# Kernel tuning notes

Hardware: AMD Instinct MI355X
Metric: run time of the kernel (lower is better)

## Reference

```python
import jax, jax.numpy as jnp
import numpy as np

B, T, C, H, E, K = 4, 1024, 1024, 16, 8, 2
HID = 4 * C

def _ln(x, g, b, eps=1e-5):
    m = jnp.mean(x, -1, keepdims=True)
    v = jnp.mean((x - m) ** 2, -1, keepdims=True)
    return (x - m) * jax.lax.rsqrt(v + eps) * g + b

def setup_inputs() -> dict:
    key = jax.random.key(0)
    ks = jax.random.split(key, 8)
    s = 0.02
    return {
        "x": jax.random.normal(ks[0], (B, T, C), jnp.float32),
        "attention_mask": jnp.ones((B, T), jnp.int32),
        "Wq": jax.random.normal(ks[1], (C, C), jnp.float32) * s,
        "bq": jnp.zeros((C,), jnp.float32),
        "Wk": jax.random.normal(ks[2], (C, C), jnp.float32) * s,
        "bk": jnp.zeros((C,), jnp.float32),
        "Wv": jax.random.normal(ks[3], (C, C), jnp.float32) * s,
        "bv": jnp.zeros((C,), jnp.float32),
        "Wo": jax.random.normal(ks[4], (C, C), jnp.float32) * s,
        "bo": jnp.zeros((C,), jnp.float32),
        "ln1_g": jnp.ones((C,), jnp.float32),
        "ln1_b": jnp.zeros((C,), jnp.float32),
        "ln2_g": jnp.ones((C,), jnp.float32),
        "ln2_b": jnp.zeros((C,), jnp.float32),
        "Wr": jax.random.normal(ks[5], (C, E), jnp.float32) * s,
        "br": jnp.zeros((E,), jnp.float32),
        "W1": jax.random.normal(ks[6], (E, C, HID), jnp.float32) * s,
        "b1": jnp.zeros((E, HID), jnp.float32),
        "W2": jax.random.normal(ks[7], (E, HID, C), jnp.float32) * s,
        "b2": jnp.zeros((E, C), jnp.float32),
    }

def reference(x, attention_mask, Wq, bq, Wk, bk, Wv, bv, Wo, bo,
              ln1_g, ln1_b, ln2_g, ln2_b, Wr, br, W1, b1, W2, b2):
    b, t, c = x.shape
    d = c // H
    # --- multi-head self-attention with causal + padding mask ---
    q = (x @ Wq + bq).reshape(b, t, H, d).transpose(0, 2, 1, 3)  # bhtd
    k = (x @ Wk + bk).reshape(b, t, H, d).transpose(0, 2, 1, 3)
    v = (x @ Wv + bv).reshape(b, t, H, d).transpose(0, 2, 1, 3)
    scores = jnp.einsum('bhqd,bhkd->bhqk', q, k) * (1.0 / jnp.sqrt(jnp.float32(d)))
    causal = jnp.tril(jnp.ones((t, t), bool))[None, None]            # [1,1,T,T]
    mask = causal & (attention_mask[:, None, None, :] > 0)          # [B,1,T,T]
    scores = jnp.where(mask, scores, jnp.float32(-1e9))
    attn = jax.nn.softmax(scores, axis=-1)
    o = jnp.einsum('bhqk,bhkd->bhqd', attn, v).transpose(0, 2, 1, 3).reshape(b, t, c)
    mha_out = o @ Wo + bo
    x1 = _ln(x + mha_out, ln1_g, ln1_b)
    # --- sparse MoE: router -> top-k gates -> expert MLPs -> combine ---
    logits = x1 @ Wr + br                               # [B,T,E]
    probs = jax.nn.softmax(logits, axis=-1)
    _, topi = jax.lax.top_k(logits, K)                  # [B,T,K]
    emask = jnp.any(topi[..., None] == jnp.arange(E), axis=-2)  # [B,T,E] bool
    gates = jax.nn.softmax(jnp.where(emask, logits, jnp.float32(-1e9)), axis=-1)
    h = jax.nn.relu(jnp.einsum('btc,ech->bteh', x1, W1) + b1)   # [B,T,E,4C]
    oe = jnp.einsum('bteh,ehc->btec', h, W2) + b2               # [B,T,E,C]
    moe_out = jnp.einsum('btec,bte->btc', oe, gates)
    # load-balancing aux loss: E * sum(mean_prob_e * frac_routed_e)
    importance = probs.mean((0, 1))
    load = emask.astype(probs.dtype).mean((0, 1))
    lb_loss = jnp.float32(E) * jnp.sum(importance * load)
    x2 = _ln(x1 + moe_out, ln2_g, ln2_b)
    return (x2, lb_loss)
```

## Files before the change

kernel.cpp:

```cpp
#include <hip/hip_runtime.h>
#include <hip/hip_bf16.h>

typedef unsigned short u16;
typedef unsigned int u32;
typedef unsigned long long u64;
typedef __attribute__((ext_vector_type(8))) _Float16 half8;
typedef __attribute__((ext_vector_type(8))) short short8;
typedef __attribute__((ext_vector_type(4))) float f32x4;
typedef __attribute__((ext_vector_type(16))) float f32x16;
typedef __attribute__((ext_vector_type(4))) int int4v;

#define DEVI __device__ __forceinline__

static constexpr int TOK = 4096;
static constexpr int CCD = 1024;
static constexpr int HIDD = 4096;
static constexpr int MAXMT = 32;

DEVI u16 f2bf(float f) {
  u32 u = __builtin_bit_cast(u32, f);
  u32 r = (u + 0x7fffu + ((u >> 16) & 1u)) >> 16;
  return (u16)r;
}
DEVI u32 pkh2(_Float16 a, _Float16 b) {
  u16 ua = __builtin_bit_cast(u16, a), ub = __builtin_bit_cast(u16, b);
  return (u32)ua | ((u32)ub << 16);
}
union H8U { u32 u[4]; half8 h; };
DEVI f32x16 zero16() { f32x16 z;
#pragma unroll
  for (int i = 0; i < 16; ++i) z[i] = 0.f;
  return z; }
DEVI f32x4 zero4() { f32x4 z;
#pragma unroll
  for (int i = 0; i < 4; ++i) z[i] = 0.f;
  return z; }

DEVI void gload16(const void* g, void* l) {
  __builtin_amdgcn_global_load_lds(
      (const __attribute__((address_space(1))) void*)g,
      (__attribute__((address_space(3))) void*)l, 16, 0, 0);
}

__global__ __launch_bounds__(256) void cast_split_kernel(
    const float* __restrict__ x, _Float16* __restrict__ xh, _Float16* __restrict__ xl) {
  int i = blockIdx.x * 256 + threadIdx.x;
  float4 v = ((const float4*)x)[i];
  _Float16 h0 = (_Float16)v.x, h1 = (_Float16)v.y, h2 = (_Float16)v.z, h3 = (_Float16)v.w;
  _Float16 l0 = (_Float16)(v.x - (float)h0), l1 = (_Float16)(v.y - (float)h1);
  _Float16 l2 = (_Float16)(v.z - (float)h2), l3 = (_Float16)(v.w - (float)h3);
  ((uint2*)xh)[i] = make_uint2(pkh2(h0, h1), pkh2(h2, h3));
  ((uint2*)xl)[i] = make_uint2(pkh2(l0, l1), pkh2(l2, l3));
}

__global__ __launch_bounds__(256) void trans_split_kernel(
    const float* __restrict__ in, _Float16* __restrict__ oh, _Float16* __restrict__ ol,
    int K, int N) {
  __shared__ float tile[32][33];
  int k0 = blockIdx.x * 32, n0 = blockIdx.y * 32;
  int tx = threadIdx.x & 31, ty = threadIdx.x >> 5;
#pragma unroll
  for (int i = 0; i < 4; ++i) { int r = ty + i * 8; tile[r][tx] = in[(size_t)(k0 + r) * N + n0 + tx]; }
  __syncthreads();
#pragma unroll
  for (int i = 0; i < 4; ++i) {
    int r = ty + i * 8;
    float v = tile[tx][r];
    _Float16 h = (_Float16)v;
    oh[(size_t)(n0 + r) * K + k0 + tx] = h;
    ol[(size_t)(n0 + r) * K + k0 + tx] = (_Float16)(v - (float)h);
  }
}

__global__ __launch_bounds__(256) void trans_bf16_kernel(
    const float* __restrict__ in, u16* __restrict__ ob, int K, int N) {
  __shared__ float tile[32][33];
  in += (size_t)blockIdx.z * K * N;
  ob += (size_t)blockIdx.z * K * N;
  int k0 = blockIdx.x * 32, n0 = blockIdx.y * 32;
  int tx = threadIdx.x & 31, ty = threadIdx.x >> 5;
#pragma unroll
  for (int i = 0; i < 4; ++i) { int r = ty + i * 8; tile[r][tx] = in[(size_t)(k0 + r) * N + n0 + tx]; }
  __syncthreads();
#pragma unroll
  for (int i = 0; i < 4; ++i) {
    int r = ty + i * 8;
    ob[(size_t)(n0 + r) * K + k0 + tx] = f2bf(tile[tx][r]);
  }
}

__global__ __launch_bounds__(256) void vtrans_kernel(
    const _Float16* __restrict__ vh, const _Float16* __restrict__ vl,
    _Float16* __restrict__ vth, _Float16* __restrict__ vtl) {
  __shared__ _Float16 t0[32][33], t1[32][33];
  size_t base = (size_t)blockIdx.z * 65536;
  int r0 = blockIdx.x * 32;
  int c0 = blockIdx.y * 32;
  int tx = threadIdx.x & 31, ty = threadIdx.x >> 5;
#pragma unroll
  for (int i = 0; i < 4; ++i) {
    int r = ty + i * 8;
    t0[r][tx] = vh[base + (size_t)(r0 + r) * 64 + c0 + tx];
    t1[r][tx] = vl[base + (size_t)(r0 + r) * 64 + c0 + tx];
  }
  __syncthreads();
#pragma unroll
  for (int i = 0; i < 4; ++i) {
    int r = ty + i * 8;
    vth[base + (size_t)(c0 + r) * 1024 + r0 + tx] = t0[tx][r];
    vtl[base + (size_t)(c0 + r) * 1024 + r0 + tx] = t1[tx][r];
  }
}

template <int EPI>
__global__ __launch_bounds__(256) void gemm_f16x3_kernel(
    const _Float16* __restrict__ Ah, const _Float16* __restrict__ Al,
    const _Float16* __restrict__ Bh, const _Float16* __restrict__ Bl,
    const float* __restrict__ bias0, const float* __restrict__ bias1, const float* __restrict__ bias2,
    _Float16* __restrict__ q_h, _Float16* __restrict__ q_l,
    _Float16* __restrict__ k_h, _Float16* __restrict__ k_l,
    _Float16* __restrict__ v_h, _Float16* __restrict__ v_l,
    float* __restrict__ outf, int M, int N, int K) {
  __shared__ __align__(16) _Float16 sA[2][128 * 64];
  __shared__ __align__(16) _Float16 sB[2][128 * 64];
  const int tid = threadIdx.x;
  const int mt = blockIdx.x, nt = blockIdx.y;
  const int lane = tid & 63, wv = tid >> 6;
  const int wm = wv >> 1, wn = wv & 1;
  f32x4 acc[4][4];
#pragma unroll
  for (int m = 0; m < 4; ++m)
#pragma unroll
    for (int n = 0; n < 4; ++n) acc[m][n] = zero4();

  const _Float16* aS[4]; const _Float16* bS[4];
#pragma unroll
  for (int j = 0; j < 4; ++j) {
    int flat = j * 256 + tid;
    int row = flat >> 3, sg = flat & 7, s = sg ^ (row & 7), g = s >> 1, hl = s & 1;
    aS[j] = (hl ? Al : Ah) + (size_t)(mt * 128 + row) * K + g * 8;
    bS[j] = (hl ? Bl : Bh) + (size_t)(nt * 128 + row) * K + g * 8;
  }

  const int nkt = K >> 5;
#pragma unroll
  for (int j = 0; j < 4; ++j) gload16(aS[j], (char*)sA[0] + (j * 256 + tid) * 16);
#pragma unroll
  for (int j = 0; j < 4; ++j) gload16(bS[j], (char*)sB[0] + (j * 256 + tid) * 16);

  for (int kt = 0; kt < nkt; ++kt) {
    const int cur = kt & 1;
    if (kt + 1 < nkt) {
#pragma unroll
      for (int j = 0; j < 4; ++j) gload16(aS[j] + (kt + 1) * 32, (char*)sA[cur ^ 1] + (j * 256 + tid) * 16);
#pragma unroll
      for (int j = 0; j < 4; ++j) gload16(bS[j] + (kt + 1) * 32, (char*)sB[cur ^ 1] + (j * 256 + tid) * 16);
      asm volatile("s_waitcnt vmcnt(8)" ::: "memory");
    } else {
      asm volatile("s_waitcnt vmcnt(0)" ::: "memory");
    }
    __builtin_amdgcn_s_barrier();
    const int g2 = (lane >> 4) << 1;
    half8 bhf[4], blf[4];
#pragma unroll
    for (int n = 0; n < 4; ++n) {
      int row = wn * 64 + n * 16 + (lane & 15);
      const char* base = (const char*)sB[cur] + row * 128;
      bhf[n] = *(const half8*)(base + (((g2) ^ (row & 7)) << 4));
      blf[n] = *(const half8*)(base + (((g2 + 1) ^ (row & 7)) << 4));
    }
    __builtin_amdgcn_s_setprio(1);
#pragma unroll
    for (int m = 0; m < 4; ++m) {
      int row = wm * 64 + m * 16 + (lane & 15);
      const char* base = (const char*)sA[cur] + row * 128;
      half8 af = *(const half8*)(base + (((g2) ^ (row & 7)) << 4));
      half8 alf = *(const half8*)(base + (((g2 + 1) ^ (row & 7)) << 4));
#pragma unroll
      for (int n = 0; n < 4; ++n) {
        acc[m][n] = __builtin_amdgcn_mfma_f32_16x16x32_f16(af, bhf[n], acc[m][n], 0, 0, 0);
        acc[m][n] = __builtin_amdgcn_mfma_f32_16x16x32_f16(af, blf[n], acc[m][n], 0, 0, 0);
        acc[m][n] = __builtin_amdgcn_mfma_f32_16x16x32_f16(alf, bhf[n], acc[m][n], 0, 0, 0);
      }
    }
    __builtin_amdgcn_s_setprio(0);
    __builtin_amdgcn_s_barrier();
  }
#pragma unroll
  for (int m = 0; m < 4; ++m) {
    int lrow = wm * 64 + m * 16 + ((lane >> 4) << 2);
#pragma unroll
    for (int n = 0; n < 4; ++n) {
      int gcol = nt * 128 + wn * 64 + n * 16 + (lane & 15);
      f32x4 a = acc[m][n];
#pragma unroll
      for (int j = 0; j < 4; ++j) {
        int grow = mt * 128 + lrow + j;
        float v = a[j];
        if (EPI == 0) {
          int sec = gcol >> 10, cc = gcol & 1023;
          v += (sec == 0 ? bias0[cc] : (sec == 1 ? bias1[cc] : bias2[cc]));
          int hh = cc >> 6, dd = cc & 63;
          int bb = grow >> 10, tt = grow & 1023;
          size_t dst = (((size_t)(bb * 16 + hh)) * 1024 + tt) * 64 + dd;
          _Float16 hi = (_Float16)v;
          _Float16 lo = (_Float16)(v - (float)hi);
          if (sec == 0) { q_h[dst] = hi; q_l[dst] = lo; }
          else if (sec == 1) { k_h[dst] = hi; k_l[dst] = lo; }
          else { v_h[dst] = hi; v_l[dst] = lo; }
        } else {
          v += bias0[gcol];
          outf[(size_t)grow * N + gcol] = v;
        }
      }
    }
  }
}

__global__ __launch_bounds__(256) void attn_kernel(
    const _Float16* __restrict__ qhp, const _Float16* __restrict__ qlp,
    const _Float16* __restrict__ khp, const _Float16* __restrict__ klp,
    const _Float16* __restrict__ vth, const _Float16* __restrict__ vtl,
    const int* __restrict__ amask,
    _Float16* __restrict__ ohp, _Float16* __restrict__ olp) {
  const int lane = threadIdx.x & 63;
  const int wv = threadIdx.x >> 6;
  const int bh = blockIdx.x >> 3;
  const int qblk = ((blockIdx.x & 7) << 2) | wv;
  const int b = bh >> 4, hh = bh & 15;
  const int q0 = qblk * 32;
  const int qln = lane & 31;
  const int qq = q0 + qln;
  const int hf = lane >> 5;
  __shared__ float lmadd[1024];
  for (int i = threadIdx.x; i < 1024; i += 256) lmadd[i] = (amask[b * 1024 + i] > 0) ? 0.f : -1e9f;
  __syncthreads();

  size_t qoff = ((size_t)bh * 1024 + qq) * 64 + hf * 8;
  half8 qfh[4], qfl[4];
#pragma unroll
  for (int d = 0; d < 4; ++d) {
    qfh[d] = *(const half8*)(qhp + qoff + d * 16);
    qfl[d] = *(const half8*)(qlp + qoff + d * 16);
  }
  f32x16 o0 = zero16(), o1 = zero16();
  float mrun = -3.0e38f, lsum = 0.f;
  const float LOG2E = 1.44269504088896f;

  for (int kb = 0; kb <= qblk; ++kb) {
    size_t koff = ((size_t)bh * 1024 + kb * 32 + qln) * 64 + hf * 8;
    f32x16 s = zero16();
#pragma unroll
    for (int d = 0; d < 4; ++d) {
      half8 kfh = *(const half8*)(khp + koff + d * 16);
      half8 kfl = *(const half8*)(klp + koff + d * 16);
      s = __builtin_amdgcn_mfma_f32_32x32x16_f16(kfh, qfh[d], s, 0, 0, 0);
      s = __builtin_amdgcn_mfma_f32_32x32x16_f16(kfh, qfl[d], s, 0, 0, 0);
      s = __builtin_amdgcn_mfma_f32_32x32x16_f16(kfl, qfh[d], s, 0, 0, 0);
    }
    float sc[16];
#pragma unroll
    for (int r = 0; r < 16; ++r) {
      int krow = (r & 3) + ((r >> 2) << 3) + (hf << 2);
      int key = kb * 32 + krow;
      sc[r] = s[r] * 0.125f + lmadd[key];
    }
    if (kb == qblk) {
#pragma unroll
      for (int r = 0; r < 16; ++r) {
        int krow = (r & 3) + ((r >> 2) << 3) + (hf << 2);
        if (kb * 32 + krow > qq) sc[r] = -1e9f;
      }
    }
    float pm = sc[0];
#pragma unroll
    for (int r = 1; r < 16; ++r) pm = fmaxf(pm, sc[r]);
    pm = fmaxf(pm, __shfl_xor(pm, 32));
    float mnew = fmaxf(mrun, pm);
    float aold = exp2f((mrun - mnew) * LOG2E);
    float p[16]; float psum = 0.f;
#pragma unroll
    for (int r = 0; r < 16; ++r) { p[r] = exp2f((sc[r] - mnew) * LOG2E); psum += p[r]; }
    lsum = lsum * aold + psum;
#pragma unroll
    for (int j = 0; j < 16; ++j) { o0[j] *= aold; o1[j] *= aold; }
    mrun = mnew;
    u32 hd[8], ld[8];
#pragma unroll
    for (int i = 0; i < 8; ++i) {
      _Float16 h0 = (_Float16)p[2 * i], h1 = (_Float16)p[2 * i + 1];
      hd[i] = pkh2(h0, h1);
      ld[i] = pkh2((_Float16)(p[2 * i] - (float)h0), (_Float16)(p[2 * i + 1] - (float)h1));
    }
    auto mkfrag = [&](u32 d0, u32 d1, u32 d2, u32 d3) -> half8 {
      u32 e0 = (u32)__shfl_xor((int)d0, 32);
      u32 e1 = (u32)__shfl_xor((int)d1, 32);
      u32 e2 = (u32)__shfl_xor((int)d2, 32);
      u32 e3 = (u32)__shfl_xor((int)d3, 32);
      H8U t;
      t.u[0] = hf ? e2 : d0;
      t.u[1] = hf ? e3 : d1;
      t.u[2] = hf ? d2 : e0;
      t.u[3] = hf ? d3 : e1;
      return t.h;
    };
    half8 pbh0 = mkfrag(hd[0], hd[1], hd[2], hd[3]);
    half8 pbl0 = mkfrag(ld[0], ld[1], ld[2], ld[3]);
    half8 pbh1 = mkfrag(hd[4], hd[5], hd[6], hd[7]);
    half8 pbl1 = mkfrag(ld[4], ld[5], ld[6], ld[7]);
    size_t vb = ((size_t)bh * 64 + qln) * 1024 + kb * 32 + hf * 8;
    half8 vh00 = *(const half8*)(vth + vb);
    half8 vh01 = *(const half8*)(vth + vb + 16);
    half8 vh10 = *(const half8*)(vth + vb + 32 * 1024);
    half8 vh11 = *(const half8*)(vth + vb + 32 * 1024 + 16);
    half8 vl00 = *(const half8*)(vtl + vb);
    half8 vl01 = *(const half8*)(vtl + vb + 16);
    half8 vl10 = *(const half8*)(vtl + vb + 32 * 1024);
    half8 vl11 = *(const half8*)(vtl + vb + 32 * 1024 + 16);
    o0 = __builtin_amdgcn_mfma_f32_32x32x16_f16(vh00, pbh0, o0, 0, 0, 0);
    o0 = __builtin_amdgcn_mfma_f32_32x32x16_f16(vh00, pbl0, o0, 0, 0, 0);
    o0 = __builtin_amdgcn_mfma_f32_32x32x16_f16(vl00, pbh0, o0, 0, 0, 0);
    o0 = __builtin_amdgcn_mfma_f32_32x32x16_f16(vh01, pbh1, o0, 0, 0, 0);
    o0 = __builtin_amdgcn_mfma_f32_32x32x16_f16(vh01, pbl1, o0, 0, 0, 0);
    o0 = __builtin_amdgcn_mfma_f32_32x32x16_f16(vl01, pbh1, o0, 0, 0, 0);
    o1 = __builtin_amdgcn_mfma_f32_32x32x16_f16(vh10, pbh0, o1, 0, 0, 0);
    o1 = __builtin_amdgcn_mfma_f32_32x32x16_f16(vh10, pbl0, o1, 0, 0, 0);
    o1 = __builtin_amdgcn_mfma_f32_32x32x16_f16(vl10, pbh0, o1, 0, 0, 0);
    o1 = __builtin_amdgcn_mfma_f32_32x32x16_f16(vh11, pbh1, o1, 0, 0, 0);
    o1 = __builtin_amdgcn_mfma_f32_32x32x16_f16(vh11, pbl1, o1, 0, 0, 0);
    o1 = __builtin_amdgcn_mfma_f32_32x32x16_f16(vl11, pbh1, o1, 0, 0, 0);
  }
  lsum += __shfl_xor(lsum, 32);
  float inv = 1.f / lsum;
  size_t obase = ((size_t)(b * 1024 + qq)) * 1024 + hh * 64;
#pragma unroll
  for (int dt = 0; dt < 2; ++dt) {
#pragma unroll
    for (int c = 0; c < 4; ++c) {
      int dloc = dt * 32 + c * 8 + hf * 4;
      float v0, v1, v2, v3;
      if (dt == 0) { v0 = o0[4 * c] * inv; v1 = o0[4 * c + 1] * inv; v2 = o0[4 * c + 2] * inv; v3 = o0[4 * c + 3] * inv; }
      else { v0 = o1[4 * c] * inv; v1 = o1[4 * c + 1] * inv; v2 = o1[4 * c + 2] * inv; v3 = o1[4 * c + 3] * inv; }
      _Float16 h0 = (_Float16)v0, h1 = (_Float16)v1, h2 = (_Float16)v2, h3 = (_Float16)v3;
      *(uint2*)(ohp + obase + dloc) = make_uint2(pkh2(h0, h1), pkh2(h2, h3));
      *(uint2*)(olp + obase + dloc) = make_uint2(
          pkh2((_Float16)(v0 - (float)h0), (_Float16)(v1 - (float)h1)),
          pkh2((_Float16)(v2 - (float)h2), (_Float16)(v3 - (float)h3)));
    }
  }
}

__global__ __launch_bounds__(256) void ln1_kernel(
    const float* __restrict__ x, const float* __restrict__ mha,
    const float* __restrict__ gam, const float* __restrict__ bet,
    float* __restrict__ x1f, u16* __restrict__ x1b) {
  int t = blockIdx.x, tid = threadIdx.x;
  const float* xr = x + (size_t)t * 1024;
  const float* mr = mha + (size_t)t * 1024;
  float v[4], s = 0.f, ss = 0.f;
#pragma unroll
  for (int i = 0; i < 4; ++i) { int c = tid + i * 256; float a = xr[c] + mr[c]; v[i] = a; s += a; ss += a * a; }
#pragma unroll
  for (int o = 32; o; o >>= 1) { s += __shfl_xor(s, o); ss += __shfl_xor(ss, o); }
  __shared__ float rs[4], rss[4];
  int wv = tid >> 6;
  if ((tid & 63) == 0) { rs[wv] = s; rss[wv] = ss; }
  __syncthreads();
  s = rs[0] + rs[1] + rs[2] + rs[3];
  ss = rss[0] + rss[1] + rss[2] + rss[3];
  float mean = s * (1.f / 1024.f);
  float var = ss * (1.f / 1024.f) - mean * mean;
  float rstd = rsqrtf(var + 1e-5f);
#pragma unroll
  for (int i = 0; i < 4; ++i) {
    int c = tid + i * 256;
    float y = (v[i] - mean) * rstd * gam[c] + bet[c];
    x1f[(size_t)t * 1024 + c] = y;
    x1b[(size_t)t * 1024 + c] = f2bf(y);
  }
}

__global__ __launch_bounds__(256) void router_kernel(
    const float* __restrict__ x1f, const float* __restrict__ Wr, const float* __restrict__ br,
    int* __restrict__ eids, float* __restrict__ gatesv, float* __restrict__ probbuf) {
  int wv = threadIdx.x >> 6, lane = threadIdx.x & 63;
  int t = blockIdx.x * 4 + wv;
  const float* xr = x1f + (size_t)t * 1024;
  float acc[8];
#pragma unroll
  for (int e = 0; e < 8; ++e) acc[e] = 0.f;
  for (int c = lane; c < 1024; c += 64) {
    float xv = xr[c];
    const float* wr = Wr + c * 8;
#pragma unroll
    for (int e = 0; e < 8; ++e) acc[e] += xv * wr[e];
  }
#pragma unroll
  for (int e = 0; e < 8; ++e) {
#pragma unroll
    for (int o = 32; o; o >>= 1) acc[e] += __shfl_xor(acc[e], o);
    acc[e] += br[e];
  }
  if (lane == 0) {
    float mx = acc[0];
#pragma unroll
    for (int e = 1; e < 8; ++e) mx = fmaxf(mx, acc[e]);
    float pe[8], se = 0.f;
#pragma unroll
    for (int e = 0; e < 8; ++e) { pe[e] = expf(acc[e] - mx); se += pe[e]; }
    float inv = 1.f / se;
#pragma unroll
    for (int e = 0; e < 8; ++e) probbuf[(size_t)t * 8 + e] = pe[e] * inv;
    int i0 = 0;
#pragma unroll
    for (int e = 1; e < 8; ++e) if (acc[e] > acc[i0]) i0 = e;
    int i1 = -1;
#pragma unroll
    for (int e = 0; e < 8; ++e) if (e != i0 && (i1 < 0 || acc[e] > acc[i1])) i1 = e;
    float m2 = fmaxf(acc[i0], acc[i1]);
    float g0 = expf(acc[i0] - m2), g1 = expf(acc[i1] - m2);
    float gs = 1.f / (g0 + g1);
    eids[t * 2] = i0; eids[t * 2 + 1] = i1;
    gatesv[t * 2] = g0 * gs; gatesv[t * 2 + 1] = g1 * gs;
  }
}

__global__ __launch_bounds__(256) void count_offs_kernel(
    const int* __restrict__ eids, int* __restrict__ counts, int* __restrict__ offs) {
  __shared__ int lc[8];
  if (threadIdx.x < 8) lc[threadIdx.x] = 0;
  __syncthreads();
  for (int i = threadIdx.x; i < TOK * 2; i += 256) atomicAdd(&lc[eids[i]], 1);
  __syncthreads();
  if (threadIdx.x == 0) {
    int s = 0;
#pragma unroll
    for (int e = 0; e < 8; ++e) { counts[e] = lc[e]; offs[e] = s; s += lc[e]; }
    offs[8] = s;
  }
}

__global__ __launch_bounds__(256) void scatter_kernel(
    const int* __restrict__ eids, const int* __restrict__ offs, int* __restrict__ cursor,
    int* __restrict__ tlist, int* __restrict__ invx) {
  int t = blockIdx.x * 256 + threadIdx.x;
  int lane = threadIdx.x & 63;
#pragma unroll
  for (int s = 0; s < 2; ++s) {
    int e = eids[t * 2 + s];
#pragma unroll
    for (int ex = 0; ex < 8; ++ex) {
      u64 m = __ballot(e == ex);
      if (e == ex) {
        int leader = __ffsll((long long)m) - 1;
        int rank = __popcll(m & ((1ull << lane) - 1ull));
        int base = 0;
        if (lane == leader) base = atomicAdd(&cursor[ex], __popcll(m));
        base = __shfl(base, leader);
        int idx = offs[ex] + base + rank;
        tlist[idx] = t;
        invx[t * 2 + s] = idx;
      }
    }
  }
}

template <int EPI>
__global__ __launch_bounds__(256) void gemm_bf16_kernel(
    const u16* __restrict__ Abase, const u16* __restrict__ Bbase, const float* __restrict__ bias,
    u16* __restrict__ outb, float* __restrict__ outf,
    const int* __restrict__ tlist, const int* __restrict__ offs,
    int K, int N, int NTILES) {
  int bid = blockIdx.x;
  int e = bid / (MAXMT * NTILES);
  int rem = bid % (MAXMT * NTILES);
  int mt = rem / NTILES, nt = rem % NTILES;
  int mstart = offs[e], mend = offs[e + 1];
  int ne = mend - mstart;
  if (mt * 128 >= ne) return;
  const u16* Bt = Bbase + (size_t)e * N * K;
  const float* bvec = bias + (size_t)e * N;
  __shared__ __align__(16) u16 sA[2][128 * 64];
  __shared__ __align__(16) u16 sB[2][128 * 64];
  const int tid = threadIdx.x;
  const int lane = tid & 63, wv = tid >> 6;
  const int wm = wv >> 1, wn = wv & 1;
  f32x4 acc[4][4];
#pragma unroll
  for (int m = 0; m < 4; ++m)
#pragma unroll
    for (int n = 0; n < 4; ++n) acc[m][n] = zero4();

  const u16* aS[4]; const u16* bS[4];
#pragma unroll
  for (int j = 0; j < 4; ++j) {
    int flat = j * 256 + tid;
    int row = flat >> 3, sg = flat & 7, g = sg ^ (row & 7);
    int rl = mt * 128 + row;
    if (rl >= ne) rl = ne - 1;
    size_t arow = (EPI == 2) ? (size_t)tlist[mstart + rl] : (size_t)(mstart + rl);
    aS[j] = Abase + arow * K + g * 8;
    bS[j] = Bt + (size_t)(nt * 128 + row) * K + g * 8;
  }

  const int nkt = K >> 6;
#pragma unroll
  for (int j = 0; j < 4; ++j) gload16(aS[j], (char*)sA[0] + (j * 256 + tid) * 16);
#pragma unroll
  for (int j = 0; j < 4; ++j) gload16(bS[j], (char*)sB[0] + (j * 256 + tid) * 16);

  for (int kt = 0; kt < nkt; ++kt) {
    const int cur = kt & 1;
    if (kt + 1 < nkt) {
#pragma unroll
      for (int j = 0; j < 4; ++j) gload16(aS[j] + (kt + 1) * 64, (char*)sA[cur ^ 1] + (j * 256 + tid) * 16);
#pragma unroll
      for (int j = 0; j < 4; ++j) gload16(bS[j] + (kt + 1) * 64, (char*)sB[cur ^ 1] + (j * 256 + tid) * 16);
      asm volatile("s_waitcnt vmcnt(8)" ::: "memory");
    } else {
      asm volatile("s_waitcnt vmcnt(0)" ::: "memory");
    }
    __builtin_amdgcn_s_barrier();
#pragma unroll
    for (int kk = 0; kk < 2; ++kk) {
      int gg = kk * 4 + (lane >> 4);
      short8 bfr[4];
#pragma unroll
      for (int n = 0; n < 4; ++n) {
        int row = wn * 64 + n * 16 + (lane & 15);
        bfr[n] = *(const short8*)((const char*)sB[cur] + row * 128 + ((gg ^ (row & 7)) << 4));
      }
      __builtin_amdgcn_s_setprio(1);
#pragma unroll
      for (int m = 0; m < 4; ++m) {
        int row = wm * 64 + m * 16 + (lane & 15);
        short8 afr = *(const short8*)((const char*)sA[cur] + row * 128 + ((gg ^ (row & 7)) << 4));
#pragma unroll
        for (int n = 0; n < 4; ++n)
          acc[m][n] = __builtin_amdgcn_mfma_f32_16x16x32_bf16(afr, bfr[n], acc[m][n], 0, 0, 0);
      }
      __builtin_amdgcn_s_setprio(0);
    }
    __builtin_amdgcn_s_barrier();
  }
#pragma unroll
  for (int m = 0; m < 4; ++m) {
    int lrow = wm * 64 + m * 16 + ((lane >> 4) << 2);
#pragma unroll
    for (int n = 0; n < 4; ++n) {
      int col = nt * 128 + wn * 64 + n * 16 + (lane & 15);
      f32x4 a = acc[m][n];
#pragma unroll
      for (int j = 0; j < 4; ++j) {
        int rl = mt * 128 + lrow + j;
        if (rl < ne) {
          size_t pair = (size_t)(mstart + rl);
          float v = a[j] + bvec[col];
          if (EPI == 2) { v = fmaxf(v, 0.f); outb[pair * N + col] = f2bf(v); }
          else outf[pair * N + col] = v;
        }
      }
    }
  }
}

__global__ __launch_bounds__(256) void ln2_kernel(
    const float* __restrict__ x1f, const float* __restrict__ oe,
    const int* __restrict__ invx, const float* __restrict__ gatesv,
    const float* __restrict__ gam, const float* __restrict__ bet, float* __restrict__ out) {
  int t = blockIdx.x, tid = threadIdx.x;
  int i0 = invx[t * 2], i1 = invx[t * 2 + 1];
  float g0 = gatesv[t * 2], g1 = gatesv[t * 2 + 1];
  const float* r0 = oe + (size_t)i0 * 1024;
  const float* r1 = oe + (size_t)i1 * 1024;
  const float* xr = x1f + (size_t)t * 1024;
  float v[4], s = 0.f, ss = 0.f;
#pragma unroll
  for (int i = 0; i < 4; ++i) {
    int c = tid + i * 256;
    float a = xr[c] + g0 * r0[c] + g1 * r1[c];
    v[i] = a; s += a; ss += a * a;
  }
#pragma unroll
  for (int o = 32; o; o >>= 1) { s += __shfl_xor(s, o); ss += __shfl_xor(ss, o); }
  __shared__ float rs[4], rss[4];
  int wv = tid >> 6;
  if ((tid & 63) == 0) { rs[wv] = s; rss[wv] = ss; }
  __syncthreads();
  s = rs[0] + rs[1] + rs[2] + rs[3];
  ss = rss[0] + rss[1] + rss[2] + rss[3];
  float mean = s * (1.f / 1024.f);
  float var = ss * (1.f / 1024.f) - mean * mean;
  float rstd = rsqrtf(var + 1e-5f);
#pragma unroll
  for (int i = 0; i < 4; ++i) {
    int c = tid + i * 256;
    out[(size_t)t * 1024 + c] = (v[i] - mean) * rstd * gam[c] + bet[c];
  }
}

__global__ __launch_bounds__(256) void loss_kernel(
    const float* __restrict__ probbuf, const int* __restrict__ counts,
    float* __restrict__ out) {
  __shared__ float ps[256][8];
  float a[8];
#pragma unroll
  for (int e = 0; e < 8; ++e) a[e] = 0.f;
  for (int r = threadIdx.x; r < TOK; r += 256) {
#pragma unroll
    for (int e = 0; e < 8; ++e) a[e] += probbuf[(size_t)r * 8 + e];
  }
#pragma unroll
  for (int e = 0; e < 8; ++e) ps[threadIdx.x][e] = a[e];
  __syncthreads();
  if (threadIdx.x == 0) {
    float s = 0.f;
#pragma unroll
    for (int e = 0; e < 8; ++e) {
      float imp = 0.f;
      for (int i = 0; i < 256; ++i) imp += ps[i][e];
      s += (imp * (1.f / 4096.f)) * ((float)counts[e] * (1.f / 4096.f));
    }
    out[0] = 8.f * s;
  }
}

extern "C" void kernel_launch(void* const* d_in, const int* in_sizes, int n_in,
                              void* d_out, int out_size, void* d_ws, size_t ws_size,
                              hipStream_t stream) {
  const float* x = (const float*)d_in[0];
  const int* amask = (const int*)d_in[1];
  const float* Wq = (const float*)d_in[2]; const float* bq = (const float*)d_in[3];
  const float* Wk = (const float*)d_in[4]; const float* bk = (const float*)d_in[5];
  const float* Wv = (const float*)d_in[6]; const float* bv = (const float*)d_in[7];
  const float* Wo = (const float*)d_in[8]; const float* bo = (const float*)d_in[9];
  const float* g1 = (const float*)d_in[10]; const float* be1 = (const float*)d_in[11];
  const float* g2 = (const float*)d_in[12]; const float* be2 = (const float*)d_in[13];
  const float* Wr = (const float*)d_in[14]; const float* br = (const float*)d_in[15];
  const float* W1 = (const float*)d_in[16]; const float* b1 = (const float*)d_in[17];
  const float* W2 = (const float*)d_in[18]; const float* b2 = (const float*)d_in[19];
  float* out = (float*)d_out;

  char* w = (char*)d_ws;
  auto alloc = [&](size_t bytes) -> char* {
    char* p = w; w += (bytes + 255) & ~(size_t)255; return p;
  };
  _Float16* xsh = (_Float16*)alloc((size_t)TOK * CCD * 2);
  _Float16* xsl = (_Float16*)alloc((size_t)TOK * CCD * 2);
  _Float16* wqh = (_Float16*)alloc((size_t)3072 * 1024 * 2);
  _Float16* wql = (_Float16*)alloc((size_t)3072 * 1024 * 2);
  _Float16* woh = (_Float16*)alloc((size_t)1024 * 1024 * 2);
  _Float16* wol = (_Float16*)alloc((size_t)1024 * 1024 * 2);
  _Float16* qhi = (_Float16*)alloc((size_t)TOK * CCD * 2);
  _Float16* qlo = (_Float16*)alloc((size_t)TOK * CCD * 2);
  _Float16* khi = (_Float16*)alloc((size_t)TOK * CCD * 2);
  _Float16* klo = (_Float16*)alloc((size_t)TOK * CCD * 2);
  _Float16* vhi = (_Float16*)alloc((size_t)TOK * CCD * 2);
  _Float16* vlo = (_Float16*)alloc((size_t)TOK * CCD * 2);
  _Float16* vthi = (_Float16*)alloc((size_t)TOK * CCD * 2);
  _Float16* vtlo = (_Float16*)alloc((size_t)TOK * CCD * 2);
  _Float16* ohi = (_Float16*)alloc((size_t)TOK * CCD * 2);
  _Float16* olo = (_Float16*)alloc((size_t)TOK * CCD * 2);
  float* mha = (float*)alloc((size_t)TOK * CCD * 4);
  float* x1f = (float*)alloc((size_t)TOK * CCD * 4);
  u16* x1b = (u16*)alloc((size_t)TOK * CCD * 2);
  u16* w1t = (u16*)alloc((size_t)8 * HIDD * CCD * 2);
  u16* w2t = (u16*)alloc((size_t)8 * CCD * HIDD * 2);
  u16* hbuf = (u16*)alloc((size_t)8192 * HIDD * 2);
  float* oe = (float*)alloc((size_t)8192 * CCD * 4);
  float* probbuf = (float*)alloc((size_t)TOK * 8 * 4);
  int* eids = (int*)alloc(TOK * 2 * 4);
  float* gatesv = (float*)alloc(TOK * 2 * 4);
  int* invx = (int*)alloc(TOK * 2 * 4);
  int* tlist = (int*)alloc(8192 * 4);
  char* ctrl = alloc(4096);
  int* counts = (int*)ctrl;
  int* cursor = counts + 8;
  int* offs = counts + 16;

  hipMemsetAsync(ctrl, 0, 256, stream);

  cast_split_kernel<<<4096, 256, 0, stream>>>(x, xsh, xsl);
  trans_split_kernel<<<dim3(32, 32), 256, 0, stream>>>(Wq, wqh, wql, 1024, 1024);
  trans_split_kernel<<<dim3(32, 32), 256, 0, stream>>>(Wk, wqh + (size_t)1024 * 1024, wql + (size_t)1024 * 1024, 1024, 1024);
  trans_split_kernel<<<dim3(32, 32), 256, 0, stream>>>(Wv, wqh + (size_t)2048 * 1024, wql + (size_t)2048 * 1024, 1024, 1024);
  trans_split_kernel<<<dim3(32, 32), 256, 0, stream>>>(Wo, woh, wol, 1024, 1024);
  trans_bf16_kernel<<<dim3(32, 128, 8), 256, 0, stream>>>(W1, w1t, 1024, 4096);
  trans_bf16_kernel<<<dim3(128, 32, 8), 256, 0, stream>>>(W2, w2t, 4096, 1024);

  gemm_f16x3_kernel<0><<<dim3(32, 24), 256, 0, stream>>>(
      xsh, xsl, wqh, wql, bq, bk, bv,
      qhi, qlo, khi, klo, vhi, vlo, nullptr, 4096, 3072, 1024);
  vtrans_kernel<<<dim3(32, 2, 64), 256, 0, stream>>>(vhi, vlo, vthi, vtlo);
  attn_kernel<<<512, 256, 0, stream>>>(qhi, qlo, khi, klo, vthi, vtlo, amask, ohi, olo);
  gemm_f16x3_kernel<1><<<dim3(32, 8), 256, 0, stream>>>(
      ohi, olo, woh, wol, bo, nullptr, nullptr,
      nullptr, nullptr, nullptr, nullptr, nullptr, nullptr, mha, 4096, 1024, 1024);
  ln1_kernel<<<4096, 256, 0, stream>>>(x, mha, g1, be1, x1f, x1b);
  router_kernel<<<1024, 256, 0, stream>>>(x1f, Wr, br, eids, gatesv, probbuf);
  count_offs_kernel<<<1, 256, 0, stream>>>(eids, counts, offs);
  scatter_kernel<<<16, 256, 0, stream>>>(eids, offs, cursor, tlist, invx);
  gemm_bf16_kernel<2><<<8 * MAXMT * 32, 256, 0, stream>>>(
      x1b, w1t, b1, hbuf, nullptr, tlist, offs, 1024, 4096, 32);
  gemm_bf16_kernel<3><<<8 * MAXMT * 8, 256, 0, stream>>>(
      hbuf, w2t, b2, nullptr, oe, nullptr, offs, 4096, 1024, 8);
  ln2_kernel<<<4096, 256, 0, stream>>>(x1f, oe, invx, gatesv, g2, be2, out);
  loss_kernel<<<1, 256, 0, stream>>>(probbuf, counts, out + (size_t)TOK * CCD);
}
```

Baseline: 821.5 us.

## Use 512-thread GEMM blocks and split-K the expert down-projection

Both GEMM kernels now run 8 waves per 128x128 tile instead of 4, so each wave owns a 64x32 sub-tile with fewer accumulators. The intent is more waves per CU to hide latency. The second expert GEMM is split along K into two halves via blockIdx.y, which doubles its grid to fill more CUs. Each half writes its own partial output, and ln2 sums the two partials. The partial buffer reuses the qhi..qlo region instead of a fresh allocation, which costs extra memory traffic for the partials and depends on that aliasing being safe.

```diff
diff --git a/kernel.cpp b/kernel.cpp
--- a/kernel.cpp
+++ b/kernel.cpp
@@ -113,7 +113,7 @@
 }
 
 template <int EPI>
-__global__ __launch_bounds__(256) void gemm_f16x3_kernel(
+__global__ __launch_bounds__(512, 4) void gemm_f16x3_kernel(
     const _Float16* __restrict__ Ah, const _Float16* __restrict__ Al,
     const _Float16* __restrict__ Bh, const _Float16* __restrict__ Bl,
     const float* __restrict__ bias0, const float* __restrict__ bias1, const float* __restrict__ bias2,
@@ -126,17 +126,17 @@
   const int tid = threadIdx.x;
   const int mt = blockIdx.x, nt = blockIdx.y;
   const int lane = tid & 63, wv = tid >> 6;
-  const int wm = wv >> 1, wn = wv & 1;
-  f32x4 acc[4][4];
+  const int wm = wv >> 2, wn = wv & 3;
+  f32x4 acc[4][2];
 #pragma unroll
   for (int m = 0; m < 4; ++m)
 #pragma unroll
-    for (int n = 0; n < 4; ++n) acc[m][n] = zero4();
-
-  const _Float16* aS[4]; const _Float16* bS[4];
-#pragma unroll
-  for (int j = 0; j < 4; ++j) {
-    int flat = j * 256 + tid;
+    for (int n = 0; n < 2; ++n) acc[m][n] = zero4();
+
+  const _Float16* aS[2]; const _Float16* bS[2];
+#pragma unroll
+  for (int j = 0; j < 2; ++j) {
+    int flat = j * 512 + tid;
     int row = flat >> 3, sg = flat & 7, s = sg ^ (row & 7), g = s >> 1, hl = s & 1;
     aS[j] = (hl ? Al : Ah) + (size_t)(mt * 128 + row) * K + g * 8;
     bS[j] = (hl ? Bl : Bh) + (size_t)(nt * 128 + row) * K + g * 8;
@@ -144,27 +144,27 @@
 
   const int nkt = K >> 5;
 #pragma unroll
-  for (int j = 0; j < 4; ++j) gload16(aS[j], (char*)sA[0] + (j * 256 + tid) * 16);
-#pragma unroll
-  for (int j = 0; j < 4; ++j) gload16(bS[j], (char*)sB[0] + (j * 256 + tid) * 16);
+  for (int j = 0; j < 2; ++j) gload16(aS[j], (char*)sA[0] + (j * 512 + tid) * 16);
+#pragma unroll
+  for (int j = 0; j < 2; ++j) gload16(bS[j], (char*)sB[0] + (j * 512 + tid) * 16);
 
   for (int kt = 0; kt < nkt; ++kt) {
     const int cur = kt & 1;
     if (kt + 1 < nkt) {
 #pragma unroll
-      for (int j = 0; j < 4; ++j) gload16(aS[j] + (kt + 1) * 32, (char*)sA[cur ^ 1] + (j * 256 + tid) * 16);
-#pragma unroll
-      for (int j = 0; j < 4; ++j) gload16(bS[j] + (kt + 1) * 32, (char*)sB[cur ^ 1] + (j * 256 + tid) * 16);
-      asm volatile("s_waitcnt vmcnt(8)" ::: "memory");
+      for (int j = 0; j < 2; ++j) gload16(aS[j] + (kt + 1) * 32, (char*)sA[cur ^ 1] + (j * 512 + tid) * 16);
+#pragma unroll
+      for (int j = 0; j < 2; ++j) gload16(bS[j] + (kt + 1) * 32, (char*)sB[cur ^ 1] + (j * 512 + tid) * 16);
+      asm volatile("s_waitcnt vmcnt(4)" ::: "memory");
     } else {
       asm volatile("s_waitcnt vmcnt(0)" ::: "memory");
     }
     __builtin_amdgcn_s_barrier();
     const int g2 = (lane >> 4) << 1;
-    half8 bhf[4], blf[4];
-#pragma unroll
-    for (int n = 0; n < 4; ++n) {
-      int row = wn * 64 + n * 16 + (lane & 15);
+    half8 bhf[2], blf[2];
+#pragma unroll
+    for (int n = 0; n < 2; ++n) {
+      int row = wn * 32 + n * 16 + (lane & 15);
       const char* base = (const char*)sB[cur] + row * 128;
       bhf[n] = *(const half8*)(base + (((g2) ^ (row & 7)) << 4));
       blf[n] = *(const half8*)(base + (((g2 + 1) ^ (row & 7)) << 4));
@@ -177,7 +177,7 @@
       half8 af = *(const half8*)(base + (((g2) ^ (row & 7)) << 4));
       half8 alf = *(const half8*)(base + (((g2 + 1) ^ (row & 7)) << 4));
 #pragma unroll
-      for (int n = 0; n < 4; ++n) {
+      for (int n = 0; n < 2; ++n) {
         acc[m][n] = __builtin_amdgcn_mfma_f32_16x16x32_f16(af, bhf[n], acc[m][n], 0, 0, 0);
         acc[m][n] = __builtin_amdgcn_mfma_f32_16x16x32_f16(af, blf[n], acc[m][n], 0, 0, 0);
         acc[m][n] = __builtin_amdgcn_mfma_f32_16x16x32_f16(alf, bhf[n], acc[m][n], 0, 0, 0);
@@ -190,8 +190,8 @@
   for (int m = 0; m < 4; ++m) {
     int lrow = wm * 64 + m * 16 + ((lane >> 4) << 2);
 #pragma unroll
-    for (int n = 0; n < 4; ++n) {
-      int gcol = nt * 128 + wn * 64 + n * 16 + (lane & 15);
+    for (int n = 0; n < 2; ++n) {
+      int gcol = nt * 128 + wn * 32 + n * 16 + (lane & 15);
       f32x4 a = acc[m][n];
 #pragma unroll
       for (int j = 0; j < 4; ++j) {
@@ -466,11 +466,11 @@
 }
 
 template <int EPI>
-__global__ __launch_bounds__(256) void gemm_bf16_kernel(
+__global__ __launch_bounds__(512, 4) void gemm_bf16_kernel(
     const u16* __restrict__ Abase, const u16* __restrict__ Bbase, const float* __restrict__ bias,
     u16* __restrict__ outb, float* __restrict__ outf,
     const int* __restrict__ tlist, const int* __restrict__ offs,
-    int K, int N, int NTILES) {
+    int K, int ldA, int N, int NTILES) {
   int bid = blockIdx.x;
   int e = bid / (MAXMT * NTILES);
   int rem = bid % (MAXMT * NTILES);
@@ -478,45 +478,47 @@
   int mstart = offs[e], mend = offs[e + 1];
   int ne = mend - mstart;
   if (mt * 128 >= ne) return;
-  const u16* Bt = Bbase + (size_t)e * N * K;
+  const int half = blockIdx.y;
+  const int kOff = half * K;
+  const u16* Bt = Bbase + (size_t)e * N * ldA;
   const float* bvec = bias + (size_t)e * N;
   __shared__ __align__(16) u16 sA[2][128 * 64];
   __shared__ __align__(16) u16 sB[2][128 * 64];
   const int tid = threadIdx.x;
   const int lane = tid & 63, wv = tid >> 6;
-  const int wm = wv >> 1, wn = wv & 1;
-  f32x4 acc[4][4];
+  const int wm = wv >> 2, wn = wv & 3;
+  f32x4 acc[4][2];
 #pragma unroll
   for (int m = 0; m < 4; ++m)
 #pragma unroll
-    for (int n = 0; n < 4; ++n) acc[m][n] = zero4();
-
-  const u16* aS[4]; const u16* bS[4];
-#pragma unroll
-  for (int j = 0; j < 4; ++j) {
-    int flat = j * 256 + tid;
+    for (int n = 0; n < 2; ++n) acc[m][n] = zero4();
+
+  const u16* aS[2]; const u16* bS[2];
+#pragma unroll
+  for (int j = 0; j < 2; ++j) {
+    int flat = j * 512 + tid;
     int row = flat >> 3, sg = flat & 7, g = sg ^ (row & 7);
     int rl = mt * 128 + row;
     if (rl >= ne) rl = ne - 1;
     size_t arow = (EPI == 2) ? (size_t)tlist[mstart + rl] : (size_t)(mstart + rl);
-    aS[j] = Abase + arow * K + g * 8;
-    bS[j] = Bt + (size_t)(nt * 128 + row) * K + g * 8;
+    aS[j] = Abase + arow * ldA + kOff + g * 8;
+    bS[j] = Bt + (size_t)(nt * 128 + row) * ldA + kOff + g * 8;
   }
 
   const int nkt = K >> 6;
 #pragma unroll
-  for (int j = 0; j < 4; ++j) gload16(aS[j], (char*)sA[0] + (j * 256 + tid) * 16);
-#pragma unroll
-  for (int j = 0; j < 4; ++j) gload16(bS[j], (char*)sB[0] + (j * 256 + tid) * 16);
+  for (int j = 0; j < 2; ++j) gload16(aS[j], (char*)sA[0] + (j * 512 + tid) * 16);
+#pragma unroll
+  for (int j = 0; j < 2; ++j) gload16(bS[j], (char*)sB[0] + (j * 512 + tid) * 16);
 
   for (int kt = 0; kt < nkt; ++kt) {
     const int cur = kt & 1;
     if (kt + 1 < nkt) {
 #pragma unroll
-      for (int j = 0; j < 4; ++j) gload16(aS[j] + (kt + 1) * 64, (char*)sA[cur ^ 1] + (j * 256 + tid) * 16);
-#pragma unroll
-      for (int j = 0; j < 4; ++j) gload16(bS[j] + (kt + 1) * 64, (char*)sB[cur ^ 1] + (j * 256 + tid) * 16);
-      asm volatile("s_waitcnt vmcnt(8)" ::: "memory");
+      for (int j = 0; j < 2; ++j) gload16(aS[j] + (kt + 1) * 64, (char*)sA[cur ^ 1] + (j * 512 + tid) * 16);
+#pragma unroll
+      for (int j = 0; j < 2; ++j) gload16(bS[j] + (kt + 1) * 64, (char*)sB[cur ^ 1] + (j * 512 + tid) * 16);
+      asm volatile("s_waitcnt vmcnt(4)" ::: "memory");
     } else {
       asm volatile("s_waitcnt vmcnt(0)" ::: "memory");
     }
@@ -524,10 +526,10 @@
 #pragma unroll
     for (int kk = 0; kk < 2; ++kk) {
       int gg = kk * 4 + (lane >> 4);
-      short8 bfr[4];
-#pragma unroll
-      for (int n = 0; n < 4; ++n) {
-        int row = wn * 64 + n * 16 + (lane & 15);
+      short8 bfr[2];
+#pragma unroll
+      for (int n = 0; n < 2; ++n) {
+        int row = wn * 32 + n * 16 + (lane & 15);
         bfr[n] = *(const short8*)((const char*)sB[cur] + row * 128 + ((gg ^ (row & 7)) << 4));
       }
       __builtin_amdgcn_s_setprio(1);
@@ -536,7 +538,7 @@
         int row = wm * 64 + m * 16 + (lane & 15);
         short8 afr = *(const short8*)((const char*)sA[cur] + row * 128 + ((gg ^ (row & 7)) << 4));
 #pragma unroll
-        for (int n = 0; n < 4; ++n)
+        for (int n = 0; n < 2; ++n)
           acc[m][n] = __builtin_amdgcn_mfma_f32_16x16x32_bf16(afr, bfr[n], acc[m][n], 0, 0, 0);
       }
       __builtin_amdgcn_s_setprio(0);
@@ -547,17 +549,17 @@
   for (int m = 0; m < 4; ++m) {
     int lrow = wm * 64 + m * 16 + ((lane >> 4) << 2);
 #pragma unroll
-    for (int n = 0; n < 4; ++n) {
-      int col = nt * 128 + wn * 64 + n * 16 + (lane & 15);
+    for (int n = 0; n < 2; ++n) {
+      int col = nt * 128 + wn * 32 + n * 16 + (lane & 15);
       f32x4 a = acc[m][n];
 #pragma unroll
       for (int j = 0; j < 4; ++j) {
         int rl = mt * 128 + lrow + j;
         if (rl < ne) {
           size_t pair = (size_t)(mstart + rl);
-          float v = a[j] + bvec[col];
+          float v = a[j] + ((EPI == 2 || half == 0) ? bvec[col] : 0.f);
           if (EPI == 2) { v = fmaxf(v, 0.f); outb[pair * N + col] = f2bf(v); }
-          else outf[pair * N + col] = v;
+          else outf[((size_t)half * 8192 + pair) * N + col] = v;
         }
       }
     }
@@ -571,14 +573,16 @@
   int t = blockIdx.x, tid = threadIdx.x;
   int i0 = invx[t * 2], i1 = invx[t * 2 + 1];
   float g0 = gatesv[t * 2], g1 = gatesv[t * 2 + 1];
-  const float* r0 = oe + (size_t)i0 * 1024;
-  const float* r1 = oe + (size_t)i1 * 1024;
+  const float* r0a = oe + (size_t)i0 * 1024;
+  const float* r0b = oe + (size_t)(8192 + i0) * 1024;
+  const float* r1a = oe + (size_t)i1 * 1024;
+  const float* r1b = oe + (size_t)(8192 + i1) * 1024;
   const float* xr = x1f + (size_t)t * 1024;
   float v[4], s = 0.f, ss = 0.f;
 #pragma unroll
   for (int i = 0; i < 4; ++i) {
     int c = tid + i * 256;
-    float a = xr[c] + g0 * r0[c] + g1 * r1[c];
+    float a = xr[c] + g0 * (r0a[c] + r0b[c]) + g1 * (r1a[c] + r1b[c]);
     v[i] = a; s += a; ss += a * a;
   }
 #pragma unroll
@@ -667,7 +671,6 @@
   u16* w1t = (u16*)alloc((size_t)8 * HIDD * CCD * 2);
   u16* w2t = (u16*)alloc((size_t)8 * CCD * HIDD * 2);
   u16* hbuf = (u16*)alloc((size_t)8192 * HIDD * 2);
-  float* oe = (float*)alloc((size_t)8192 * CCD * 4);
   float* probbuf = (float*)alloc((size_t)TOK * 8 * 4);
   int* eids = (int*)alloc(TOK * 2 * 4);
   float* gatesv = (float*)alloc(TOK * 2 * 4);
@@ -677,6 +680,7 @@
   int* counts = (int*)ctrl;
   int* cursor = counts + 8;
   int* offs = counts + 16;
+  float* oe = (float*)qhi;
 
   hipMemsetAsync(ctrl, 0, 256, stream);
 
@@ -688,22 +692,22 @@
   trans_bf16_kernel<<<dim3(32, 128, 8), 256, 0, stream>>>(W1, w1t, 1024, 4096);
   trans_bf16_kernel<<<dim3(128, 32, 8), 256, 0, stream>>>(W2, w2t, 4096, 1024);
 
-  gemm_f16x3_kernel<0><<<dim3(32, 24), 256, 0, stream>>>(
+  gemm_f16x3_kernel<0><<<dim3(32, 24), 512, 0, stream>>>(
       xsh, xsl, wqh, wql, bq, bk, bv,
       qhi, qlo, khi, klo, vhi, vlo, nullptr, 4096, 3072, 1024);
   vtrans_kernel<<<dim3(32, 2, 64), 256, 0, stream>>>(vhi, vlo, vthi, vtlo);
   attn_kernel<<<512, 256, 0, stream>>>(qhi, qlo, khi, klo, vthi, vtlo, amask, ohi, olo);
-  gemm_f16x3_kernel<1><<<dim3(32, 8), 256, 0, stream>>>(
+  gemm_f16x3_kernel<1><<<dim3(32, 8), 512, 0, stream>>>(
       ohi, olo, woh, wol, bo, nullptr, nullptr,
       nullptr, nullptr, nullptr, nullptr, nullptr, nullptr, mha, 4096, 1024, 1024);
   ln1_kernel<<<4096, 256, 0, stream>>>(x, mha, g1, be1, x1f, x1b);
   router_kernel<<<1024, 256, 0, stream>>>(x1f, Wr, br, eids, gatesv, probbuf);
   count_offs_kernel<<<1, 256, 0, stream>>>(eids, counts, offs);
   scatter_kernel<<<16, 256, 0, stream>>>(eids, offs, cursor, tlist, invx);
-  gemm_bf16_kernel<2><<<8 * MAXMT * 32, 256, 0, stream>>>(
-      x1b, w1t, b1, hbuf, nullptr, tlist, offs, 1024, 4096, 32);
-  gemm_bf16_kernel<3><<<8 * MAXMT * 8, 256, 0, stream>>>(
-      hbuf, w2t, b2, nullptr, oe, nullptr, offs, 4096, 1024, 8);
+  gemm_bf16_kernel<2><<<dim3(8 * MAXMT * 32, 1), 512, 0, stream>>>(
+      x1b, w1t, b1, hbuf, nullptr, tlist, offs, 1024, 1024, 4096, 32);
+  gemm_bf16_kernel<3><<<dim3(8 * MAXMT * 8, 2), 512, 0, stream>>>(
+      hbuf, w2t, b2, nullptr, oe, nullptr, offs, 2048, 4096, 1024, 8);
   ln2_kernel<<<4096, 256, 0, stream>>>(x1f, oe, invx, gatesv, g2, be2, out);
   loss_kernel<<<1, 256, 0, stream>>>(probbuf, counts, out + (size_t)TOK * CCD);
 }
```

Result: faster. 749.7 us (-8.7%).
